# Kernel optimization log

Measured on AMD Instinct MI355X. Metric: run time of the kernel, lower is better.

## Reference

```python
import jax, jax.numpy as jnp
import numpy as np

B, V, C, D = 32, 64, 32, 256
VOCAB = 20000
NUM_T = 1000


def _run_lstm(x, Wih, Whh, b):
    # x: [T, B, H_in]; torch-style single-layer LSTM with zero initial state
    T, Bb, _ = x.shape
    H = Whh.shape[1]
    def step(carry, xt):
        h, c = carry
        z = xt @ Wih.T + h @ Whh.T + b
        i, f, g, o = jnp.split(z, 4, axis=-1)
        c = jax.nn.sigmoid(f) * c + jax.nn.sigmoid(i) * jnp.tanh(g)
        h = jax.nn.sigmoid(o) * jnp.tanh(c)
        return (h, c), h
    h0 = jnp.zeros((Bb, H), x.dtype)
    _, ys = jax.lax.scan(step, (h0, h0), x)
    return ys


def _forward(input_seqs, masks, lengths, seq_time_step, code_masks, emb, WQ1, WK1,
             decay, initial, lstm_Wih, lstm_Whh, lstm_b, hs_Wih, hs_Whh, hs_b,
             whk_W, whk_b, w1_W, w1_b, w2_W, w2_b, fuse_W, fuse_b, lab_W, lab_b,
             betas, Wdiff, diffusion_time_t, normal_noise):
    Bb, Vv, Cc = input_seqs.shape
    tok = input_seqs.reshape(-1, Cc)                      # [B*V, C]
    x = emb[tok]                                          # [B*V, C, D]
    q = x @ WQ1.T
    k = x @ WK1.T
    dp = jnp.einsum('bcd,bed->bce', q, k)                 # [B*V, C, C]
    cm = code_masks.reshape(-1, Cc)
    dp = dp - cm[:, None, :] - cm[:, :, None]
    sp = jax.nn.softmax(dp / jnp.sqrt(jnp.float32(D)), axis=-1)
    femb = jnp.einsum('bce,bed->bcd', sp, x)              # attended code embeddings
    femb = ((cm - 1e20) / -1e20)[:, :, None] * femb       # zero out padded codes
    dec = decay[tok][..., None]                           # [B*V, C, 1]
    ini = initial[tok][..., None]
    t = seq_time_step.reshape(-1)[:, None, None]          # [B*V, 1, 1]
    gate = jax.nn.sigmoid(dec * t + ini)                  # time-decay gate
    vv = jnp.einsum('bcx,bcd->bd', gate, femb)            # [B*V, D] visit vector
    vv = vv.reshape(Bb, Vv, -1).transpose(1, 0, 2)        # [V, B, D]

    lstm_out = _run_lstm(vv, lstm_Wih, lstm_Whh, lstm_b)  # [V, B, D]
    t_lstm = lstm_out.transpose(1, 0, 2)                  # [B, V, D]
    hiddenstate = _run_lstm(lstm_out, hs_Wih, hs_Whh, hs_b).transpose(1, 0, 2)

    # Vectorized form of the original per-step python loop.
    # NOTE: the original always uses e_k = t_lstm_out[:, 0:1, :] (step 0) -- kept faithfully.
    e_k = t_lstm[:, 0:1, :]                               # [B, 1, D]
    whp = hiddenstate[:, :-1, :] @ whk_W.T + whk_b        # [B, V-1, D]
    cat = jnp.concatenate([jnp.broadcast_to(e_k, whp.shape), whp], axis=-1)
    attn = jax.nn.softmax(jnp.tanh(cat @ w1_W.T + w1_b) @ w2_W.T + w2_b, axis=-1)
    rest = e_k * attn[..., 0:1] + whp * attn[..., 1:2]
    aligned = jnp.concatenate([e_k, rest], axis=1)        # [B, V, D]

    alpha = jnp.cumprod(1.0 - betas)[diffusion_time_t][:, None, None]
    noisy = aligned * jnp.sqrt(alpha) + normal_noise * jnp.sqrt(1.0 - alpha)
    predicted_noise = noisy @ Wdiff                       # surrogate for UNetModel (source not provided)
    gen = aligned + (normal_noise - predicted_noise)

    fused = jnp.concatenate([t_lstm, gen], axis=-1) @ fuse_W.T + fuse_b   # [B, V, D]
    mask_final = (jnp.arange(Vv)[None, :] == (lengths - 1)[:, None]).astype(fused.dtype)
    final = (fused * mask_final[:, :, None]).sum(axis=1)  # select last valid visit
    return final @ lab_W.T + lab_b                        # [B, 2]


def setup_inputs() -> dict:
    key = jax.random.key(0)
    ks = jax.random.split(key, 20)
    s = 0.05
    n = lambda i, shp: jax.random.normal(ks[i], shp, jnp.float32) * s
    emb = jax.random.normal(ks[0], (VOCAB + 1, D), jnp.float32) * 0.02
    emb = emb.at[VOCAB].set(0.0)  # padding_idx row
    return {
        'input_seqs': jax.random.randint(ks[1], (B, V, C), 0, VOCAB),
        'masks': jnp.zeros((B, V), jnp.float32),
        'lengths': jax.random.randint(ks[2], (B,), 1, V + 1),
        'seq_time_step': jax.random.uniform(ks[3], (B, V), jnp.float32),
        'code_masks': jnp.zeros((B, V, C), jnp.float32),
        'emb': emb,
        'WQ1': n(4, (D, D)), 'WK1': n(5, (D, D)),
        'decay': jnp.full((VOCAB + 1,), -0.1, jnp.float32),
        'initial': jnp.full((VOCAB + 1,), 1.0, jnp.float32),
        'lstm_Wih': n(6, (4 * D, D)), 'lstm_Whh': n(7, (4 * D, D)),
        'lstm_b': jnp.zeros((4 * D,), jnp.float32),
        'hs_Wih': n(8, (4 * D, D)), 'hs_Whh': n(9, (4 * D, D)),
        'hs_b': jnp.zeros((4 * D,), jnp.float32),
        'whk_W': n(10, (D, D)), 'whk_b': jnp.zeros((D,), jnp.float32),
        'w1_W': n(11, (64, 2 * D)), 'w1_b': jnp.zeros((64,), jnp.float32),
        'w2_W': n(12, (2, 64)), 'w2_b': jnp.zeros((2,), jnp.float32),
        'fuse_W': n(13, (D, 2 * D)), 'fuse_b': jnp.zeros((D,), jnp.float32),
        'lab_W': n(14, (2, D)), 'lab_b': jnp.zeros((2,), jnp.float32),
        'betas': jnp.linspace(1e-4, 0.02, NUM_T, dtype=jnp.float32),
        'Wdiff': n(15, (D, D)),
        'diffusion_time_t': jax.random.randint(ks[16], (B,), 0, NUM_T),
        'normal_noise': jax.random.normal(ks[17], (B, V, D), jnp.float32),
    }


def reference(input_seqs, masks, lengths, seq_time_step, code_masks, emb, WQ1, WK1,
              decay, initial, lstm_Wih, lstm_Whh, lstm_b, hs_Wih, hs_Whh, hs_b,
              whk_W, whk_b, w1_W, w1_b, w2_W, w2_b, fuse_W, fuse_b, lab_W, lab_b,
              betas, Wdiff, diffusion_time_t, normal_noise):
    return _forward(input_seqs, masks, lengths, seq_time_step, code_masks, emb, WQ1, WK1,
                    decay, initial, lstm_Wih, lstm_Whh, lstm_b, hs_Wih, hs_Whh, hs_b,
                    whk_W, whk_b, w1_W, w1_b, w2_W, w2_b, fuse_W, fuse_b, lab_W, lab_b,
                    betas, Wdiff, diffusion_time_t, normal_noise)
```

## Files before the change

kernel.cpp:

```cpp
#include <hip/hip_runtime.h>
#include <hip/hip_bf16.h>
#include <cmath>

typedef __attribute__((ext_vector_type(8))) short bf16x8;
typedef __attribute__((ext_vector_type(4))) float f32x4;
typedef __attribute__((ext_vector_type(4))) int i32x4;
typedef __attribute__((ext_vector_type(2))) unsigned int u32x2;

__device__ __forceinline__ float bf2f(unsigned short u) {
    unsigned int x = ((unsigned int)u) << 16;
    return __builtin_bit_cast(float, x);
}
__device__ __forceinline__ unsigned short f2bf(float f) {
    unsigned int x = __builtin_bit_cast(unsigned int, f);
    unsigned int lsb = (x >> 16) & 1u;
    x += 0x7fffu + lsb;
    return (unsigned short)(x >> 16);
}
__device__ __forceinline__ float sigm(float z) {
    return 1.f / (1.f + __expf(-z));
}
__device__ __forceinline__ float rcpf(float x) { return __builtin_amdgcn_rcpf(x); }
__device__ __forceinline__ float sigm_f(float z) { return rcpf(1.f + __expf(-z)); }
__device__ __forceinline__ float tanh_f(float z) { return 1.f - 2.f * rcpf(1.f + __expf(2.f * z)); }

__device__ __forceinline__ long ldg_sc8l(const void* p) {
    long r;
    asm volatile("global_load_dwordx2 %0, %1, off sc1" : "=v"(r) : "v"(p) : "memory");
    return r;
}
__device__ __forceinline__ u32x2 ldg_sc_u2(const void* p) {
    u32x2 r;
    asm volatile("global_load_dwordx2 %0, %1, off sc1" : "=v"(r) : "v"(p) : "memory");
    return r;
}
__device__ __forceinline__ void stg_sc_u2(void* p, u32x2 v) {
    asm volatile("global_store_dwordx2 %0, %1, off sc1" :: "v"(p), "v"(v) : "memory");
}
__device__ __forceinline__ void stg_sc_b(void* p, int v) {
    asm volatile("global_store_byte %0, %1, off sc1" :: "v"(p), "v"(v) : "memory");
}

__global__ void __launch_bounds__(256) pack_all(
    const float* __restrict__ Whh1, const float* __restrict__ Wih2,
    const float* __restrict__ Whh2, const float* __restrict__ Wih1,
    const float* __restrict__ WQ1, const float* __restrict__ WK1,
    const float* __restrict__ betas, const int* __restrict__ dift,
    const float* __restrict__ whk_W, const float* __restrict__ fuse_W,
    const float* __restrict__ w1_W,
    long* __restrict__ Wq, float* __restrict__ cs,
    unsigned short* __restrict__ W1h, unsigned short* __restrict__ M_pk,
    float* __restrict__ alpha, int* __restrict__ flags,
    float* __restrict__ whkT, float* __restrict__ fuseT,
    float* __restrict__ w1T) {
    int blk = blockIdx.x, tid = threadIdx.x;
    if (blk < 384) {
        int R = blk * 8 + (tid >> 5);
        int mat = R >> 10;
        int n = R & 1023;
        int t32 = tid & 31;
        const float* src = (mat == 0) ? Whh1 : (mat == 1 ? Wih2 : Whh2);
        const float* rp = src + (size_t)n * 256 + t32 * 8;
        float v[8];
        float mx = 0.f;
        for (int j = 0; j < 8; ++j) { v[j] = rp[j]; mx = fmaxf(mx, fabsf(v[j])); }
        for (int m = 1; m <= 16; m <<= 1) mx = fmaxf(mx, __shfl_xor(mx, m));
        float inv = mx > 0.f ? 127.f / mx : 0.f;
        unsigned int lo = 0, hi = 0;
        for (int j = 0; j < 4; ++j) {
            int iv = __float2int_rn(v[j] * inv);
            lo |= ((unsigned int)(unsigned char)(signed char)iv) << (8 * j);
            int iv2 = __float2int_rn(v[4 + j] * inv);
            hi |= ((unsigned int)(unsigned char)(signed char)iv2) << (8 * j);
        }
        int g = n >> 8, rem = n & 255;
        int w8 = rem >> 5, dt = (rem >> 4) & 1, cc = rem & 15;
        int t8 = g * 2 + dt;
        int kb = t32 >> 2, q = t32 & 3;
        unsigned int* dst = (unsigned int*)Wq +
            ((size_t)((mat * 512 + w8 * 64 + t8 * 8 + kb) * 64) + q * 16 + cc) * 2;
        dst[0] = lo;
        dst[1] = hi;
        if (t32 == 0) cs[mat * 1024 + n] = mx / 16129.f;
    } else if (blk < 512) {
        int cch = (blk - 384) * 256 + tid;
        int nt = cch >> 9;
        int r = cch & 511;
        int kb = r >> 6;
        int lane = r & 63;
        int grow = nt * 16 + (lane & 15);
        int k0 = kb * 32 + (lane >> 4) * 8;
        const float* sp = Wih1 + (size_t)grow * 256 + k0;
        bf16x8 hi;
        for (int j = 0; j < 8; ++j) hi[j] = (short)f2bf(sp[j]);
        *reinterpret_cast<bf16x8*>(W1h + (size_t)cch * 8) = hi;
    } else if (blk == 512) {
        if (tid < 32) {
            int tb = dift[tid];
            float p = 1.f;
            for (int i = 0; i <= tb; ++i) p *= (1.f - betas[i]);
            alpha[tid] = p;
        }
    } else if (blk == 513) {
        for (int i = tid; i < 2048; i += 256) flags[i] = 0;
    } else if (blk < 578) {
        int gid = (blk - 514) * 256 + tid;
        for (int i = 0; i < 4; ++i) {
            int e = gid + i * 16384;
            int k = e >> 8, dd = e & 255;
            whkT[e] = whk_W[(size_t)dd * 256 + k];
        }
    } else if (blk < 706) {
        int gid = (blk - 578) * 256 + tid;
        for (int i = 0; i < 4; ++i) {
            int e = gid + i * 32768;
            int k = e >> 8, dd = e & 255;
            fuseT[e] = fuse_W[(size_t)dd * 512 + k];
        }
    } else if (blk < 738) {
        int gid = (blk - 706) * 256 + tid;
        for (int i = 0; i < 4; ++i) {
            int e = gid + i * 8192;
            int k = e >> 6, j = e & 63;
            w1T[e] = w1_W[(size_t)j * 512 + k];
        }
    } else {
        __shared__ unsigned short As[256][32];
        __shared__ unsigned short Bs[256][32];
        int bx = blk - 738;
        int e0 = (bx >> 3) << 5;
        int f0 = (bx & 7) << 5;
        int col = tid & 31, rr = tid >> 5;
        for (int rep = 0; rep < 32; ++rep) {
            int d = rep * 8 + rr;
            As[d][col] = f2bf(WQ1[d * 256 + e0 + col]);
            Bs[d][col] = f2bf(WK1[d * 256 + f0 + col]);
        }
        __syncthreads();
        int el = tid & 31;
        int fl0 = tid >> 5;
        for (int i = 0; i < 4; ++i) {
            int fl = fl0 + 8 * i;
            float acc = 0.f;
            for (int d = 0; d < 256; ++d)
                acc += bf2f(As[d][el]) * bf2f(Bs[d][fl]);
            int e = e0 + el, f = f0 + fl;
            int kb = e >> 5, r = (e >> 3) & 3, j = e & 7;
            int nb = f >> 4;
            int lane = (r << 4) | (f & 15);
            M_pk[(((nb * 8 + kb) * 64) + lane) * 8 + j] = f2bf(acc);
        }
    }
}

__global__ void __launch_bounds__(256) attn_bags(
    const int* __restrict__ seqs, const float* __restrict__ tstep,
    const float* __restrict__ cmask, const float* __restrict__ emb,
    const float* __restrict__ decay, const float* __restrict__ initial,
    const unsigned short* __restrict__ M_pk, float* __restrict__ vv) {
    __shared__ __align__(16) unsigned short x_bf[32 * 256];
    __shared__ __align__(16) unsigned short t1_bf[32 * 256];
    __shared__ float dp_f[32 * 33];
    __shared__ float gate_sh[32];
    __shared__ float cm_sh[32];
    __shared__ int tok_sh[32];
    __shared__ float w_sh[32];

    int bag = blockIdx.x;
    int tid = threadIdx.x;

    if (tid < 32) {
        int tok = seqs[bag * 32 + tid];
        tok_sh[tid] = tok;
        float cm = cmask[bag * 32 + tid];
        cm_sh[tid] = cm;
        float tt = tstep[bag];
        float g = sigm(decay[tok] * tt + initial[tok]);
        g *= (cm - 1e20f) / (-1e20f);
        gate_sh[tid] = g;
    }
    __syncthreads();

    for (int it = 0; it < 8; ++it) {
        int fidx = it * 256 + tid;
        int c = fidx >> 6;
        int f4 = fidx & 63;
        const float4* src = reinterpret_cast<const float4*>(emb + (size_t)tok_sh[c] * 256) + f4;
        float4 vx = *src;
        int colx = f4 * 4;
        int eidx = c * 256 + (colx ^ ((c & 7) << 3));
        ushort4 w;
        w.x = f2bf(vx.x); w.y = f2bf(vx.y); w.z = f2bf(vx.z); w.w = f2bf(vx.w);
        *reinterpret_cast<ushort4*>(&x_bf[eidx]) = w;
    }
    __syncthreads();

    int wv = tid >> 6;
    int lane = tid & 63;
    int lr = lane & 15;
    int lk = lane >> 4;

    f32x4 acc[2][4];
    for (int a = 0; a < 2; ++a)
        for (int n = 0; n < 4; ++n) acc[a][n] = (f32x4){0.f, 0.f, 0.f, 0.f};
    for (int kb = 0; kb < 8; ++kb) {
        bf16x8 afr[2];
        for (int mb = 0; mb < 2; ++mb) {
            int row = mb * 16 + lr;
            int colx = kb * 32 + lk * 8;
            afr[mb] = *reinterpret_cast<const bf16x8*>(&x_bf[row * 256 + (colx ^ ((row & 7) << 3))]);
        }
        for (int nbi = 0; nbi < 4; ++nbi) {
            int nb = wv * 4 + nbi;
            bf16x8 bfr = *reinterpret_cast<const bf16x8*>(M_pk + (((nb * 8 + kb) * 64) + lane) * 8);
            acc[0][nbi] = __builtin_amdgcn_mfma_f32_16x16x32_bf16(afr[0], bfr, acc[0][nbi], 0, 0, 0);
            acc[1][nbi] = __builtin_amdgcn_mfma_f32_16x16x32_bf16(afr[1], bfr, acc[1][nbi], 0, 0, 0);
        }
    }
    for (int mb = 0; mb < 2; ++mb)
        for (int nbi = 0; nbi < 4; ++nbi)
            for (int r = 0; r < 4; ++r) {
                int row = mb * 16 + lk * 4 + r;
                int colx = wv * 64 + nbi * 16 + lr;
                t1_bf[row * 256 + (colx ^ ((row & 7) << 3))] = f2bf(acc[mb][nbi][r]);
            }
    __syncthreads();

    {
        int mb = wv >> 1, nb2 = wv & 1;
        f32x4 dacc = (f32x4){0.f, 0.f, 0.f, 0.f};
        for (int kb = 0; kb < 8; ++kb) {
            int cola = kb * 32 + lk * 8;
            int rowa = mb * 16 + lr;
            bf16x8 afr = *reinterpret_cast<const bf16x8*>(&t1_bf[rowa * 256 + (cola ^ ((rowa & 7) << 3))]);
            int rowb = nb2 * 16 + lr;
            bf16x8 bfr = *reinterpret_cast<const bf16x8*>(&x_bf[rowb * 256 + (cola ^ ((rowb & 7) << 3))]);
            dacc = __builtin_amdgcn_mfma_f32_16x16x32_bf16(afr, bfr, dacc, 0, 0, 0);
        }
        for (int r = 0; r < 4; ++r) {
            int c = mb * 16 + lk * 4 + r;
            int e = nb2 * 16 + lr;
            dp_f[c * 33 + e] = dacc[r];
        }
    }
    __syncthreads();

    if (tid < 32) {
        int c = tid;
        float cmc = cm_sh[c];
        float lg[32];
        float mx = -1e30f;
        for (int e = 0; e < 32; ++e) {
            float l = (dp_f[c * 33 + e] - cmc - cm_sh[e]) * 0.0625f;
            lg[e] = l;
            mx = fmaxf(mx, l);
        }
        float s = 0.f;
        for (int e = 0; e < 32; ++e) { float ex = __expf(lg[e] - mx); lg[e] = ex; s += ex; }
        float inv = 1.f / s;
        for (int e = 0; e < 32; ++e) dp_f[c * 33 + e] = lg[e] * inv;
    }
    __syncthreads();
    if (tid < 32) {
        int e = tid;
        float a2 = 0.f;
        for (int c = 0; c < 32; ++c) a2 += gate_sh[c] * dp_f[c * 33 + e];
        w_sh[e] = a2;
    }
    __syncthreads();

    float accv = 0.f;
    int d = tid;
    for (int e = 0; e < 32; ++e)
        accv += w_sh[e] * bf2f(x_bf[e * 256 + (d ^ ((e & 7) << 3))]);
    vv[(size_t)bag * 256 + d] = accv;
}

__global__ void __launch_bounds__(256) x1_mfma(const float* __restrict__ vv,
                                               const unsigned short* __restrict__ W1h,
                                               const float* __restrict__ lstm_b,
                                               unsigned short* __restrict__ X1bf) {
    __shared__ __align__(16) unsigned short xs[32 * 256];
    int blk = blockIdx.x;
    int rb = blk >> 3, gb = blk & 7;
    int tid = threadIdx.x;
    for (int it = 0; it < 8; ++it) {
        int idx = it * 256 + tid;
        int row = idx >> 6, f4 = idx & 63;
        float4 v = *reinterpret_cast<const float4*>(vv + (size_t)(rb * 32 + row) * 256 + f4 * 4);
        ushort4 w;
        w.x = f2bf(v.x); w.y = f2bf(v.y); w.z = f2bf(v.z); w.w = f2bf(v.w);
        *reinterpret_cast<ushort4*>(&xs[row * 256 + ((f4 * 4) ^ ((row & 7) << 3))]) = w;
    }
    __syncthreads();
    int wv = tid >> 6, lane = tid & 63, cl = lane & 15, kh = lane >> 4;
    f32x4 acc[2][2];
    for (int n = 0; n < 2; ++n) {
        int nt = gb * 8 + wv * 2 + n;
        float bz = lstm_b[nt * 16 + cl];
        acc[n][0] = (f32x4){bz, bz, bz, bz};
        acc[n][1] = (f32x4){bz, bz, bz, bz};
    }
    #pragma unroll
    for (int kb = 0; kb < 8; ++kb) {
        int k = kb * 32 + kh * 8;
        bf16x8 a0 = *reinterpret_cast<const bf16x8*>(&xs[cl * 256 + (k ^ ((cl & 7) << 3))]);
        bf16x8 a1 = *reinterpret_cast<const bf16x8*>(&xs[(16 + cl) * 256 + (k ^ (((16 + cl) & 7) << 3))]);
        for (int n = 0; n < 2; ++n) {
            int nt = gb * 8 + wv * 2 + n;
            size_t o = ((size_t)(nt * 8 + kb) * 64 + lane) * 8;
            bf16x8 bh = *reinterpret_cast<const bf16x8*>(W1h + o);
            acc[n][0] = __builtin_amdgcn_mfma_f32_16x16x32_bf16(a0, bh, acc[n][0], 0, 0, 0);
            acc[n][1] = __builtin_amdgcn_mfma_f32_16x16x32_bf16(a1, bh, acc[n][1], 0, 0, 0);
        }
    }
    for (int n = 0; n < 2; ++n) {
        int nt = gb * 8 + wv * 2 + n;
        int g = nt * 16 + cl;
        int dX = g & 255, gt = g >> 8;
        for (int mt = 0; mt < 2; ++mt)
            for (int r = 0; r < 4; ++r) {
                int row = rb * 32 + mt * 16 + kh * 4 + r;
                int b = row >> 6, t = row & 63;
                X1bf[((size_t)t * 32 + b) * 1024 + dX * 4 + gt] = f2bf(acc[n][mt][r]);
            }
    }
}

__global__ void __launch_bounds__(512, 2) lstm_persist(
    const long* __restrict__ Wq, const float* __restrict__ cs,
    const unsigned short* __restrict__ X1bf, const float* __restrict__ hs_b,
    unsigned short* __restrict__ h1bf, unsigned short* __restrict__ h2bf,
    signed char* h1q, unsigned short* p1, int* flags) {
    int role = blockIdx.x;
    int half = role & 1;
    int kind = role >> 1;
    int tid = threadIdx.x;
    int w = tid >> 6, lane = tid & 63, c = lane & 15, q = lane >> 4;

    long wt[64];
    #pragma unroll
    for (int t8 = 0; t8 < 8; ++t8)
        #pragma unroll
        for (int kb = 0; kb < 8; ++kb)
            wt[t8 * 8 + kb] = Wq[(size_t)((kind * 512 + w * 64 + t8 * 8 + kb) * 64) + lane];
    float csv[8];
    #pragma unroll
    for (int t8 = 0; t8 < 8; ++t8) {
        int g = t8 >> 1, dt = t8 & 1;
        csv[t8] = cs[kind * 1024 + g * 256 + w * 32 + dt * 16 + c];
    }

    if (kind == 0) {
        __shared__ signed char hq[2][16][272];
        float cstate[8] = {0.f, 0.f, 0.f, 0.f, 0.f, 0.f, 0.f, 0.f};
        int B0 = half * 16 + q * 4;
        int dbase = w * 32;
        for (int t = 0; t < 64; ++t) {
            ushort4 xv[8];
            #pragma unroll
            for (int dt = 0; dt < 2; ++dt)
                #pragma unroll
                for (int r = 0; r < 4; ++r) {
                    int B = B0 + r, d = dbase + dt * 16 + c;
                    xv[dt * 4 + r] = *reinterpret_cast<const ushort4*>(
                        X1bf + ((size_t)(t * 32 + B) * 1024 + d * 4));
                }
            i32x4 acc[8];
            #pragma unroll
            for (int i = 0; i < 8; ++i) acc[i] = (i32x4){0, 0, 0, 0};
            if (t > 0) {
                int pb = (t - 1) & 1;
                long a[8];
                #pragma unroll
                for (int kb = 0; kb < 8; ++kb)
                    a[kb] = *reinterpret_cast<const long*>(&hq[pb][c][kb * 32 + q * 8]);
                #pragma unroll
                for (int t8 = 0; t8 < 8; ++t8)
                    #pragma unroll
                    for (int kb = 0; kb < 8; ++kb)
                        acc[t8] = __builtin_amdgcn_mfma_i32_16x16x32_i8(
                            a[kb], wt[t8 * 8 + kb], acc[t8], 0, 0, 0);
            }
            #pragma unroll
            for (int dt = 0; dt < 2; ++dt)
                #pragma unroll
                for (int r = 0; r < 4; ++r) {
                    int idx = dt * 4 + r;
                    ushort4 x = xv[idx];
                    float zi = (float)acc[0 + dt][r] * csv[0 + dt] + bf2f(x.x);
                    float zf = (float)acc[2 + dt][r] * csv[2 + dt] + bf2f(x.y);
                    float zg = (float)acc[4 + dt][r] * csv[4 + dt] + bf2f(x.z);
                    float zo = (float)acc[6 + dt][r] * csv[6 + dt] + bf2f(x.w);
                    float cn = sigm_f(zf) * cstate[idx] + sigm_f(zi) * tanh_f(zg);
                    float hn = sigm_f(zo) * tanh_f(cn);
                    cstate[idx] = cn;
                    int B = B0 + r, d = dbase + dt * 16 + c;
                    h1bf[(size_t)(t * 32 + B) * 256 + d] = f2bf(hn);
                    int hv = __float2int_rn(hn * 127.f);
                    hq[t & 1][q * 4 + r][d] = (signed char)hv;
                    stg_sc_b(h1q + (size_t)(t * 32 + B) * 256 + d, hv);
                }
            asm volatile("s_waitcnt vmcnt(0)" ::: "memory");
            if (lane == 0)
                __hip_atomic_store(flags + t * 16 + half * 8 + w, 1,
                                   __ATOMIC_RELAXED, __HIP_MEMORY_SCOPE_AGENT);
            __syncthreads();
        }
    } else if (kind == 1) {
        for (int s = 0; s < 64; ++s) {
            const int* f = flags + s * 16 + half * 8;
            while (1) {
                int v = 1;
                if (lane < 8)
                    v = __hip_atomic_load(f + lane, __ATOMIC_RELAXED, __HIP_MEMORY_SCOPE_AGENT);
                if (__all(v != 0)) break;
                __builtin_amdgcn_s_sleep(1);
            }
            __builtin_amdgcn_sched_barrier(0);
            const signed char* hb = h1q + (size_t)(s * 32 + half * 16) * 256;
            long a[8];
            #pragma unroll
            for (int kb = 0; kb < 8; ++kb)
                a[kb] = ldg_sc8l(hb + c * 256 + kb * 32 + q * 8);
            asm volatile("s_waitcnt vmcnt(0)" ::: "memory");
            __builtin_amdgcn_sched_barrier(0);
            i32x4 acc[8];
            #pragma unroll
            for (int i = 0; i < 8; ++i) acc[i] = (i32x4){0, 0, 0, 0};
            #pragma unroll
            for (int t8 = 0; t8 < 8; ++t8)
                #pragma unroll
                for (int kb = 0; kb < 8; ++kb)
                    acc[t8] = __builtin_amdgcn_mfma_i32_16x16x32_i8(
                        a[kb], wt[t8 * 8 + kb], acc[t8], 0, 0, 0);
            #pragma unroll
            for (int t8 = 0; t8 < 8; ++t8) {
                int g = t8 >> 1, dt = t8 & 1;
                int n = g * 256 + w * 32 + dt * 16 + c;
                u32x2 pv;
                pv.x = (unsigned int)f2bf((float)acc[t8][0] * csv[t8]) |
                       ((unsigned int)f2bf((float)acc[t8][1] * csv[t8]) << 16);
                pv.y = (unsigned int)f2bf((float)acc[t8][2] * csv[t8]) |
                       ((unsigned int)f2bf((float)acc[t8][3] * csv[t8]) << 16);
                stg_sc_u2(p1 + ((size_t)(s * 2 + half) * 1024 + n) * 16 + q * 4, pv);
            }
            asm volatile("s_waitcnt vmcnt(0)" ::: "memory");
            if (lane == 0)
                __hip_atomic_store(flags + 1024 + s * 16 + half * 8 + w, 1,
                                   __ATOMIC_RELAXED, __HIP_MEMORY_SCOPE_AGENT);
        }
    } else {
        __shared__ signed char hq2[2][16][272];
        float cstate[8] = {0.f, 0.f, 0.f, 0.f, 0.f, 0.f, 0.f, 0.f};
        float bias[8];
        #pragma unroll
        for (int t8 = 0; t8 < 8; ++t8) {
            int g = t8 >> 1, dt = t8 & 1;
            bias[t8] = hs_b[g * 256 + w * 32 + dt * 16 + c];
        }
        int B0 = half * 16 + q * 4;
        int dbase = w * 32;
        for (int s = 0; s < 64; ++s) {
            const int* fp = flags + 1024 + s * 16 + half * 8 + w;
            while (__hip_atomic_load(fp, __ATOMIC_RELAXED, __HIP_MEMORY_SCOPE_AGENT) == 0)
                __builtin_amdgcn_s_sleep(1);
            __builtin_amdgcn_sched_barrier(0);
            u32x2 pv[8];
            #pragma unroll
            for (int t8 = 0; t8 < 8; ++t8) {
                int g = t8 >> 1, dt = t8 & 1;
                int n = g * 256 + w * 32 + dt * 16 + c;
                pv[t8] = ldg_sc_u2(p1 + ((size_t)(s * 2 + half) * 1024 + n) * 16 + q * 4);
            }
            i32x4 acc[8];
            #pragma unroll
            for (int i = 0; i < 8; ++i) acc[i] = (i32x4){0, 0, 0, 0};
            if (s > 0) {
                int pb = (s - 1) & 1;
                long a[8];
                #pragma unroll
                for (int kb = 0; kb < 8; ++kb)
                    a[kb] = *reinterpret_cast<const long*>(&hq2[pb][c][kb * 32 + q * 8]);
                asm volatile("s_waitcnt vmcnt(0)" ::: "memory");
                __builtin_amdgcn_sched_barrier(0);
                #pragma unroll
                for (int t8 = 0; t8 < 8; ++t8)
                    #pragma unroll
                    for (int kb = 0; kb < 8; ++kb)
                        acc[t8] = __builtin_amdgcn_mfma_i32_16x16x32_i8(
                            a[kb], wt[t8 * 8 + kb], acc[t8], 0, 0, 0);
            } else {
                asm volatile("s_waitcnt vmcnt(0)" ::: "memory");
                __builtin_amdgcn_sched_barrier(0);
            }
            #pragma unroll
            for (int dt = 0; dt < 2; ++dt)
                #pragma unroll
                for (int r = 0; r < 4; ++r) {
                    int idx = dt * 4 + r;
                    float p_i = bf2f((unsigned short)((r < 2 ? pv[0 + dt].x : pv[0 + dt].y) >> ((r & 1) * 16)));
                    float p_f = bf2f((unsigned short)((r < 2 ? pv[2 + dt].x : pv[2 + dt].y) >> ((r & 1) * 16)));
                    float p_g = bf2f((unsigned short)((r < 2 ? pv[4 + dt].x : pv[4 + dt].y) >> ((r & 1) * 16)));
                    float p_o = bf2f((unsigned short)((r < 2 ? pv[6 + dt].x : pv[6 + dt].y) >> ((r & 1) * 16)));
                    float zi = (float)acc[0 + dt][r] * csv[0 + dt] + p_i + bias[0 + dt];
                    float zf = (float)acc[2 + dt][r] * csv[2 + dt] + p_f + bias[2 + dt];
                    float zg = (float)acc[4 + dt][r] * csv[4 + dt] + p_g + bias[4 + dt];
                    float zo = (float)acc[6 + dt][r] * csv[6 + dt] + p_o + bias[6 + dt];
                    float cn = sigm_f(zf) * cstate[idx] + sigm_f(zi) * tanh_f(zg);
                    float hn = sigm_f(zo) * tanh_f(cn);
                    cstate[idx] = cn;
                    int B = B0 + r, d = dbase + dt * 16 + c;
                    h2bf[(size_t)(s * 32 + B) * 256 + d] = f2bf(hn);
                    hq2[s & 1][q * 4 + r][d] = (signed char)__float2int_rn(hn * 127.f);
                }
            __syncthreads();
        }
    }
}

__global__ void __launch_bounds__(256) tail_k(
    const int* __restrict__ lengths,
    const unsigned short* __restrict__ h1, const unsigned short* __restrict__ h2,
    const float* __restrict__ whkT, const float* __restrict__ whk_b,
    const float* __restrict__ w1T, const float* __restrict__ w1_b,
    const float* __restrict__ w2_W, const float* __restrict__ w2_b,
    const float* __restrict__ fuseT, const float* __restrict__ fuse_b,
    const float* __restrict__ lab_W, const float* __restrict__ lab_b,
    const float* __restrict__ Wdiff, const float* __restrict__ alpha,
    const float* __restrict__ noise, float* __restrict__ out) {
    __shared__ float ek[256], tv[256], hs[256], whp[256], a1s[64];
    __shared__ float noisy_s[256], fin[512], fused_s[256], attn_s[2];
    int b = blockIdx.x, tid = threadIdx.x;
    int vstar = lengths[b] - 1;
    {
        ek[tid] = bf2f(h1[(size_t)b * 256 + tid]);
        tv[tid] = bf2f(h1[((size_t)vstar * 32 + b) * 256 + tid]);
        if (vstar > 0)
            hs[tid] = bf2f(h2[((size_t)(vstar - 1) * 32 + b) * 256 + tid]);
    }
    __syncthreads();

    float aligned;
    if (vstar > 0) {
        float s0 = 0.f, s1 = 0.f, s2 = 0.f, s3 = 0.f;
        for (int k = 0; k < 256; k += 4) {
            s0 += whkT[(k + 0) * 256 + tid] * hs[k + 0];
            s1 += whkT[(k + 1) * 256 + tid] * hs[k + 1];
            s2 += whkT[(k + 2) * 256 + tid] * hs[k + 2];
            s3 += whkT[(k + 3) * 256 + tid] * hs[k + 3];
        }
        whp[tid] = whk_b[tid] + s0 + s1 + s2 + s3;
        __syncthreads();
        if (tid < 64) {
            float a0 = 0.f, a1 = 0.f, a2 = 0.f, a3 = 0.f;
            for (int k = 0; k < 256; k += 4) {
                a0 += w1T[(k + 0) * 64 + tid] * ek[k + 0];
                a1 += w1T[(k + 1) * 64 + tid] * ek[k + 1];
                a2 += w1T[(k + 2) * 64 + tid] * ek[k + 2];
                a3 += w1T[(k + 3) * 64 + tid] * ek[k + 3];
            }
            for (int k = 0; k < 256; k += 4) {
                a0 += w1T[(256 + k + 0) * 64 + tid] * whp[k + 0];
                a1 += w1T[(256 + k + 1) * 64 + tid] * whp[k + 1];
                a2 += w1T[(256 + k + 2) * 64 + tid] * whp[k + 2];
                a3 += w1T[(256 + k + 3) * 64 + tid] * whp[k + 3];
            }
            a1s[tid] = tanhf(w1_b[tid] + a0 + a1 + a2 + a3);
        }
        __syncthreads();
        if (tid < 2) {
            float a3 = w2_b[tid];
            const float* wr2 = w2_W + tid * 64;
            for (int k = 0; k < 64; ++k) a3 += wr2[k] * a1s[k];
            attn_s[tid] = a3;
        }
        __syncthreads();
        float m = fmaxf(attn_s[0], attn_s[1]);
        float e0 = __expf(attn_s[0] - m), e1 = __expf(attn_s[1] - m);
        float inv = 1.f / (e0 + e1);
        aligned = ek[tid] * (e0 * inv) + whp[tid] * (e1 * inv);
    } else {
        aligned = ek[tid];
    }

    float al = alpha[b];
    float sa = sqrtf(al), sb = sqrtf(1.f - al);
    float nz = noise[((size_t)b * 64 + vstar) * 256 + tid];
    noisy_s[tid] = aligned * sa + nz * sb;
    __syncthreads();
    {
        float p0 = 0.f, p1v = 0.f, p2 = 0.f, p3 = 0.f;
        for (int k = 0; k < 256; k += 4) {
            p0 += noisy_s[k + 0] * Wdiff[(size_t)(k + 0) * 256 + tid];
            p1v += noisy_s[k + 1] * Wdiff[(size_t)(k + 1) * 256 + tid];
            p2 += noisy_s[k + 2] * Wdiff[(size_t)(k + 2) * 256 + tid];
            p3 += noisy_s[k + 3] * Wdiff[(size_t)(k + 3) * 256 + tid];
        }
        float gen = aligned + nz - (p0 + p1v + p2 + p3);
        fin[tid] = tv[tid];
        fin[256 + tid] = gen;
    }
    __syncthreads();
    {
        float f0 = 0.f, f1 = 0.f, f2 = 0.f, f3 = 0.f;
        for (int k = 0; k < 512; k += 4) {
            f0 += fuseT[(k + 0) * 256 + tid] * fin[k + 0];
            f1 += fuseT[(k + 1) * 256 + tid] * fin[k + 1];
            f2 += fuseT[(k + 2) * 256 + tid] * fin[k + 2];
            f3 += fuseT[(k + 3) * 256 + tid] * fin[k + 3];
        }
        fused_s[tid] = fuse_b[tid] + f0 + f1 + f2 + f3;
    }
    __syncthreads();
    if (tid < 2) {
        float o = lab_b[tid];
        const float* lw = lab_W + tid * 256;
        for (int k = 0; k < 256; ++k) o += lw[k] * fused_s[k];
        out[b * 2 + tid] = o;
    }
}

extern "C" void kernel_launch(void* const* d_in, const int* in_sizes, int n_in,
                              void* d_out, int out_size, void* d_ws, size_t ws_size,
                              hipStream_t stream) {
    const int*   seqs    = (const int*)  d_in[0];
    const int*   lengths = (const int*)  d_in[2];
    const float* tstep   = (const float*)d_in[3];
    const float* cmask   = (const float*)d_in[4];
    const float* emb     = (const float*)d_in[5];
    const float* WQ1     = (const float*)d_in[6];
    const float* WK1     = (const float*)d_in[7];
    const float* decay   = (const float*)d_in[8];
    const float* initial = (const float*)d_in[9];
    const float* Wih1    = (const float*)d_in[10];
    const float* Whh1    = (const float*)d_in[11];
    const float* lstm_b  = (const float*)d_in[12];
    const float* Wih2    = (const float*)d_in[13];
    const float* Whh2    = (const float*)d_in[14];
    const float* hs_b    = (const float*)d_in[15];
    const float* whk_W   = (const float*)d_in[16];
    const float* whk_b   = (const float*)d_in[17];
    const float* w1_W    = (const float*)d_in[18];
    const float* w1_b    = (const float*)d_in[19];
    const float* w2_W    = (const float*)d_in[20];
    const float* w2_b    = (const float*)d_in[21];
    const float* fuse_W  = (const float*)d_in[22];
    const float* fuse_b  = (const float*)d_in[23];
    const float* lab_W   = (const float*)d_in[24];
    const float* lab_b   = (const float*)d_in[25];
    const float* betas   = (const float*)d_in[26];
    const float* Wdiff   = (const float*)d_in[27];
    const int*   dift    = (const int*)  d_in[28];
    const float* noise   = (const float*)d_in[29];
    float* out = (float*)d_out;

    float* ws = (float*)d_ws;
    size_t off = 0;
    auto alloc = [&](size_t nfloats) { size_t r = off; off += (nfloats + 63) & ~(size_t)63; return r; };
    unsigned short* M_pk  = (unsigned short*)(ws + alloc(32768));
    float*          alpha = ws + alloc(64);
    float*          cs    = ws + alloc(3072);
    int*            flags = (int*)(ws + alloc(2048));
    float*          vv    = ws + alloc(524288);
    unsigned short* X1bf  = (unsigned short*)(ws + alloc(1048576));
    unsigned short* h1bf  = (unsigned short*)(ws + alloc(262144));
    unsigned short* h2bf  = (unsigned short*)(ws + alloc(262144));
    unsigned short* p1    = (unsigned short*)(ws + alloc(1048576));
    long*           Wq    = (long*)(ws + alloc(196608));
    unsigned short* W1h   = (unsigned short*)(ws + alloc(131072));
    float*          whkT  = ws + alloc(65536);
    float*          fuseT = ws + alloc(131072);
    float*          w1T   = ws + alloc(32768);
    signed char*    h1q   = (signed char*)vv;

    pack_all<<<802, 256, 0, stream>>>(Whh1, Wih2, Whh2, Wih1, WQ1, WK1, betas, dift,
                                      whk_W, fuse_W, w1_W,
                                      Wq, cs, W1h, M_pk, alpha, flags,
                                      whkT, fuseT, w1T);
    attn_bags<<<2048, 256, 0, stream>>>(seqs, tstep, cmask, emb, decay, initial, M_pk, vv);
    x1_mfma<<<512, 256, 0, stream>>>(vv, W1h, lstm_b, X1bf);
    lstm_persist<<<6, 512, 0, stream>>>(Wq, cs, X1bf, hs_b, h1bf, h2bf, h1q, p1, flags);
    tail_k<<<32, 256, 0, stream>>>(lengths, h1bf, h2bf, whkT, whk_b,
                                   w1T, w1_b, w2_W, w2_b, fuseT, fuse_b,
                                   lab_W, lab_b, Wdiff, alpha, noise, out);
}
```

Measured before the change: 340.9 us.

## Precompute vocab-projected embeddings and coarsen LSTM pipeline flags with packed stores

A new eprep kernel multiplies the whole embedding table (20001 rows) by M_pk once, and attn_bags then gathers the projected rows instead of running its own MFMA per bag. The persistent LSTM kernel switches to one block-wide flag per step instead of per-wave flags. The second-stage producer handles two timesteps per flag, and h1q/h1bf/h2bf are written with packed stores built through lane shuffles rather than byte and short stores. This trades about 2048×32 gathered rows of compute for a full-vocab GEMM and reduces flag polling and store count, at the cost of extra __syncthreads and coarser pipeline granularity.

```diff
diff --git a/kernel.cpp b/kernel.cpp
--- a/kernel.cpp
+++ b/kernel.cpp
@@ -36,9 +36,6 @@
 }
 __device__ __forceinline__ void stg_sc_u2(void* p, u32x2 v) {
     asm volatile("global_store_dwordx2 %0, %1, off sc1" :: "v"(p), "v"(v) : "memory");
-}
-__device__ __forceinline__ void stg_sc_b(void* p, int v) {
-    asm volatile("global_store_byte %0, %1, off sc1" :: "v"(p), "v"(v) : "memory");
 }
 
 __global__ void __launch_bounds__(256) pack_all(
@@ -102,7 +99,7 @@
             alpha[tid] = p;
         }
     } else if (blk == 513) {
-        for (int i = tid; i < 2048; i += 256) flags[i] = 0;
+        for (int i = tid; i < 4096; i += 256) flags[i] = 0;
     } else if (blk < 578) {
         int gid = (blk - 514) * 256 + tid;
         for (int i = 0; i < 4; ++i) {
@@ -153,11 +150,59 @@
     }
 }
 
+__global__ void __launch_bounds__(256) eprep(const float* __restrict__ emb,
+                                             const unsigned short* __restrict__ M_pk,
+                                             unsigned short* __restrict__ Ep) {
+    __shared__ __align__(16) unsigned short x_bf[32 * 256];
+    int v0 = blockIdx.x * 32;
+    int tid = threadIdx.x;
+    for (int it = 0; it < 8; ++it) {
+        int fidx = it * 256 + tid;
+        int cc = fidx >> 6;
+        int f4 = fidx & 63;
+        int row = v0 + cc;
+        float4 vx = make_float4(0.f, 0.f, 0.f, 0.f);
+        if (row < 20001)
+            vx = *(reinterpret_cast<const float4*>(emb + (size_t)row * 256) + f4);
+        int colx = f4 * 4;
+        ushort4 w;
+        w.x = f2bf(vx.x); w.y = f2bf(vx.y); w.z = f2bf(vx.z); w.w = f2bf(vx.w);
+        *reinterpret_cast<ushort4*>(&x_bf[cc * 256 + (colx ^ ((cc & 7) << 3))]) = w;
+    }
+    __syncthreads();
+    int wv = tid >> 6, lane = tid & 63, lr = lane & 15, lk = lane >> 4;
+    f32x4 acc[2][4];
+    for (int a = 0; a < 2; ++a)
+        for (int n = 0; n < 4; ++n) acc[a][n] = (f32x4){0.f, 0.f, 0.f, 0.f};
+    for (int kb = 0; kb < 8; ++kb) {
+        bf16x8 afr[2];
+        for (int mb = 0; mb < 2; ++mb) {
+            int row = mb * 16 + lr;
+            int colx = kb * 32 + lk * 8;
+            afr[mb] = *reinterpret_cast<const bf16x8*>(&x_bf[row * 256 + (colx ^ ((row & 7) << 3))]);
+        }
+        for (int nbi = 0; nbi < 4; ++nbi) {
+            int nb = wv * 4 + nbi;
+            bf16x8 bfr = *reinterpret_cast<const bf16x8*>(M_pk + (((nb * 8 + kb) * 64) + lane) * 8);
+            acc[0][nbi] = __builtin_amdgcn_mfma_f32_16x16x32_bf16(afr[0], bfr, acc[0][nbi], 0, 0, 0);
+            acc[1][nbi] = __builtin_amdgcn_mfma_f32_16x16x32_bf16(afr[1], bfr, acc[1][nbi], 0, 0, 0);
+        }
+    }
+    for (int mb = 0; mb < 2; ++mb)
+        for (int nbi = 0; nbi < 4; ++nbi)
+            for (int r = 0; r < 4; ++r) {
+                int row = mb * 16 + lk * 4 + r;
+                int col = wv * 64 + nbi * 16 + lr;
+                if (v0 + row < 20001)
+                    Ep[(size_t)(v0 + row) * 256 + col] = f2bf(acc[mb][nbi][r]);
+            }
+}
+
 __global__ void __launch_bounds__(256) attn_bags(
     const int* __restrict__ seqs, const float* __restrict__ tstep,
     const float* __restrict__ cmask, const float* __restrict__ emb,
     const float* __restrict__ decay, const float* __restrict__ initial,
-    const unsigned short* __restrict__ M_pk, float* __restrict__ vv) {
+    const unsigned short* __restrict__ Ep, float* __restrict__ vv) {
     __shared__ __align__(16) unsigned short x_bf[32 * 256];
     __shared__ __align__(16) unsigned short t1_bf[32 * 256];
     __shared__ float dp_f[32 * 33];
@@ -193,38 +238,19 @@
         w.x = f2bf(vx.x); w.y = f2bf(vx.y); w.z = f2bf(vx.z); w.w = f2bf(vx.w);
         *reinterpret_cast<ushort4*>(&x_bf[eidx]) = w;
     }
+    for (int it = 0; it < 4; ++it) {
+        int idx = it * 256 + tid;
+        int cc = idx >> 5;
+        int colx = (idx & 31) * 8;
+        bf16x8 e = *reinterpret_cast<const bf16x8*>(Ep + (size_t)tok_sh[cc] * 256 + colx);
+        *reinterpret_cast<bf16x8*>(&t1_bf[cc * 256 + (colx ^ ((cc & 7) << 3))]) = e;
+    }
     __syncthreads();
 
     int wv = tid >> 6;
     int lane = tid & 63;
     int lr = lane & 15;
     int lk = lane >> 4;
-
-    f32x4 acc[2][4];
-    for (int a = 0; a < 2; ++a)
-        for (int n = 0; n < 4; ++n) acc[a][n] = (f32x4){0.f, 0.f, 0.f, 0.f};
-    for (int kb = 0; kb < 8; ++kb) {
-        bf16x8 afr[2];
-        for (int mb = 0; mb < 2; ++mb) {
-            int row = mb * 16 + lr;
-            int colx = kb * 32 + lk * 8;
-            afr[mb] = *reinterpret_cast<const bf16x8*>(&x_bf[row * 256 + (colx ^ ((row & 7) << 3))]);
-        }
-        for (int nbi = 0; nbi < 4; ++nbi) {
-            int nb = wv * 4 + nbi;
-            bf16x8 bfr = *reinterpret_cast<const bf16x8*>(M_pk + (((nb * 8 + kb) * 64) + lane) * 8);
-            acc[0][nbi] = __builtin_amdgcn_mfma_f32_16x16x32_bf16(afr[0], bfr, acc[0][nbi], 0, 0, 0);
-            acc[1][nbi] = __builtin_amdgcn_mfma_f32_16x16x32_bf16(afr[1], bfr, acc[1][nbi], 0, 0, 0);
-        }
-    }
-    for (int mb = 0; mb < 2; ++mb)
-        for (int nbi = 0; nbi < 4; ++nbi)
-            for (int r = 0; r < 4; ++r) {
-                int row = mb * 16 + lk * 4 + r;
-                int colx = wv * 64 + nbi * 16 + lr;
-                t1_bf[row * 256 + (colx ^ ((row & 7) << 3))] = f2bf(acc[mb][nbi][r]);
-            }
-    __syncthreads();
 
     {
         int mb = wv >> 1, nb2 = wv & 1;
@@ -361,11 +387,9 @@
             #pragma unroll
             for (int dt = 0; dt < 2; ++dt)
                 #pragma unroll
-                for (int r = 0; r < 4; ++r) {
-                    int B = B0 + r, d = dbase + dt * 16 + c;
+                for (int r = 0; r < 4; ++r)
                     xv[dt * 4 + r] = *reinterpret_cast<const ushort4*>(
-                        X1bf + ((size_t)(t * 32 + B) * 1024 + d * 4));
-                }
+                        X1bf + ((size_t)(t * 32 + B0 + r) * 1024 + (dbase + dt * 16 + c) * 4));
             i32x4 acc[8];
             #pragma unroll
             for (int i = 0; i < 8; ++i) acc[i] = (i32x4){0, 0, 0, 0};
@@ -382,6 +406,8 @@
                         acc[t8] = __builtin_amdgcn_mfma_i32_16x16x32_i8(
                             a[kb], wt[t8 * 8 + kb], acc[t8], 0, 0, 0);
             }
+            float hnv[8];
+            unsigned int hvb[8];
             #pragma unroll
             for (int dt = 0; dt < 2; ++dt)
                 #pragma unroll
@@ -395,59 +421,86 @@
                     float cn = sigm_f(zf) * cstate[idx] + sigm_f(zi) * tanh_f(zg);
                     float hn = sigm_f(zo) * tanh_f(cn);
                     cstate[idx] = cn;
-                    int B = B0 + r, d = dbase + dt * 16 + c;
-                    h1bf[(size_t)(t * 32 + B) * 256 + d] = f2bf(hn);
+                    hnv[idx] = hn;
                     int hv = __float2int_rn(hn * 127.f);
-                    hq[t & 1][q * 4 + r][d] = (signed char)hv;
-                    stg_sc_b(h1q + (size_t)(t * 32 + B) * 256 + d, hv);
+                    hq[t & 1][q * 4 + r][dbase + dt * 16 + c] = (signed char)hv;
+                    hvb[idx] = (unsigned int)(unsigned char)(signed char)hv;
                 }
-            asm volatile("s_waitcnt vmcnt(0)" ::: "memory");
-            if (lane == 0)
-                __hip_atomic_store(flags + t * 16 + half * 8 + w, 1,
+            #pragma unroll
+            for (int dt = 0; dt < 2; ++dt)
+                #pragma unroll
+                for (int r = 0; r < 4; ++r) {
+                    unsigned int b = hvb[dt * 4 + r];
+                    unsigned int p = (unsigned int)__shfl_xor((int)b, 1);
+                    unsigned int pair = (c & 1) ? (p | (b << 8)) : (b | (p << 8));
+                    unsigned int pq = (unsigned int)__shfl_xor((int)pair, 2);
+                    unsigned int quad = (c & 2) ? (pq | (pair << 16)) : (pair | (pq << 16));
+                    unsigned int oh = (unsigned int)__shfl_xor((int)quad, 4);
+                    if ((c & 7) == 0) {
+                        u32x2 v8;
+                        v8.x = quad; v8.y = oh;
+                        stg_sc_u2(h1q + (size_t)(t * 32 + B0 + r) * 256 + dbase + dt * 16 + c, v8);
+                    }
+                }
+            #pragma unroll
+            for (int dt = 0; dt < 2; ++dt)
+                #pragma unroll
+                for (int r = 0; r < 4; ++r) {
+                    unsigned int ph = f2bf(hnv[dt * 4 + r]);
+                    unsigned int pp = (unsigned int)__shfl_xor((int)ph, 1);
+                    if (!(c & 1))
+                        *reinterpret_cast<unsigned int*>(
+                            h1bf + (size_t)(t * 32 + B0 + r) * 256 + dbase + dt * 16 + c) =
+                            ph | (pp << 16);
+                }
+            __syncthreads();
+            if (tid == 0)
+                __hip_atomic_store(flags + (t * 2 + half) * 16, 1,
                                    __ATOMIC_RELAXED, __HIP_MEMORY_SCOPE_AGENT);
-            __syncthreads();
         }
     } else if (kind == 1) {
-        for (int s = 0; s < 64; ++s) {
-            const int* f = flags + s * 16 + half * 8;
-            while (1) {
-                int v = 1;
-                if (lane < 8)
-                    v = __hip_atomic_load(f + lane, __ATOMIC_RELAXED, __HIP_MEMORY_SCOPE_AGENT);
-                if (__all(v != 0)) break;
+        for (int s2 = 0; s2 < 64; s2 += 2) {
+            const int* fp = flags + ((s2 + 1) * 2 + half) * 16;
+            while (__hip_atomic_load(fp, __ATOMIC_RELAXED, __HIP_MEMORY_SCOPE_AGENT) == 0)
                 __builtin_amdgcn_s_sleep(1);
-            }
             __builtin_amdgcn_sched_barrier(0);
-            const signed char* hb = h1q + (size_t)(s * 32 + half * 16) * 256;
-            long a[8];
-            #pragma unroll
-            for (int kb = 0; kb < 8; ++kb)
-                a[kb] = ldg_sc8l(hb + c * 256 + kb * 32 + q * 8);
+            const signed char* hb0 = h1q + (size_t)(s2 * 32 + half * 16) * 256;
+            const signed char* hb1 = h1q + (size_t)((s2 + 1) * 32 + half * 16) * 256;
+            long a[8], b[8];
+            #pragma unroll
+            for (int kb = 0; kb < 8; ++kb) {
+                a[kb] = ldg_sc8l(hb0 + c * 256 + kb * 32 + q * 8);
+                b[kb] = ldg_sc8l(hb1 + c * 256 + kb * 32 + q * 8);
+            }
             asm volatile("s_waitcnt vmcnt(0)" ::: "memory");
             __builtin_amdgcn_sched_barrier(0);
-            i32x4 acc[8];
-            #pragma unroll
-            for (int i = 0; i < 8; ++i) acc[i] = (i32x4){0, 0, 0, 0};
-            #pragma unroll
-            for (int t8 = 0; t8 < 8; ++t8)
-                #pragma unroll
-                for (int kb = 0; kb < 8; ++kb)
-                    acc[t8] = __builtin_amdgcn_mfma_i32_16x16x32_i8(
-                        a[kb], wt[t8 * 8 + kb], acc[t8], 0, 0, 0);
-            #pragma unroll
-            for (int t8 = 0; t8 < 8; ++t8) {
-                int g = t8 >> 1, dt = t8 & 1;
-                int n = g * 256 + w * 32 + dt * 16 + c;
-                u32x2 pv;
-                pv.x = (unsigned int)f2bf((float)acc[t8][0] * csv[t8]) |
-                       ((unsigned int)f2bf((float)acc[t8][1] * csv[t8]) << 16);
-                pv.y = (unsigned int)f2bf((float)acc[t8][2] * csv[t8]) |
-                       ((unsigned int)f2bf((float)acc[t8][3] * csv[t8]) << 16);
-                stg_sc_u2(p1 + ((size_t)(s * 2 + half) * 1024 + n) * 16 + q * 4, pv);
-            }
-            asm volatile("s_waitcnt vmcnt(0)" ::: "memory");
-            if (lane == 0)
-                __hip_atomic_store(flags + 1024 + s * 16 + half * 8 + w, 1,
+            #pragma unroll
+            for (int step = 0; step < 2; ++step) {
+                int s = s2 + step;
+                i32x4 acc[8];
+                #pragma unroll
+                for (int i = 0; i < 8; ++i) acc[i] = (i32x4){0, 0, 0, 0};
+                #pragma unroll
+                for (int t8 = 0; t8 < 8; ++t8)
+                    #pragma unroll
+                    for (int kb = 0; kb < 8; ++kb)
+                        acc[t8] = __builtin_amdgcn_mfma_i32_16x16x32_i8(
+                            step ? b[kb] : a[kb], wt[t8 * 8 + kb], acc[t8], 0, 0, 0);
+                #pragma unroll
+                for (int t8 = 0; t8 < 8; ++t8) {
+                    int g = t8 >> 1, dt = t8 & 1;
+                    int n = g * 256 + w * 32 + dt * 16 + c;
+                    u32x2 pv;
+                    pv.x = (unsigned int)f2bf((float)acc[t8][0] * csv[t8]) |
+                           ((unsigned int)f2bf((float)acc[t8][1] * csv[t8]) << 16);
+                    pv.y = (unsigned int)f2bf((float)acc[t8][2] * csv[t8]) |
+                           ((unsigned int)f2bf((float)acc[t8][3] * csv[t8]) << 16);
+                    stg_sc_u2(p1 + ((size_t)(s * 2 + half) * 1024 + n) * 16 + q * 4, pv);
+                }
+            }
+            __syncthreads();
+            if (tid == 0)
+                __hip_atomic_store(flags + 2048 + ((s2 >> 1) * 2 + half) * 16, 1,
                                    __ATOMIC_RELAXED, __HIP_MEMORY_SCOPE_AGENT);
         }
     } else {
@@ -462,10 +515,12 @@
         int B0 = half * 16 + q * 4;
         int dbase = w * 32;
         for (int s = 0; s < 64; ++s) {
-            const int* fp = flags + 1024 + s * 16 + half * 8 + w;
-            while (__hip_atomic_load(fp, __ATOMIC_RELAXED, __HIP_MEMORY_SCOPE_AGENT) == 0)
-                __builtin_amdgcn_s_sleep(1);
-            __builtin_amdgcn_sched_barrier(0);
+            if ((s & 1) == 0) {
+                const int* fp = flags + 2048 + ((s >> 1) * 2 + half) * 16;
+                while (__hip_atomic_load(fp, __ATOMIC_RELAXED, __HIP_MEMORY_SCOPE_AGENT) == 0)
+                    __builtin_amdgcn_s_sleep(1);
+                __builtin_amdgcn_sched_barrier(0);
+            }
             u32x2 pv[8];
             #pragma unroll
             for (int t8 = 0; t8 < 8; ++t8) {
@@ -494,6 +549,7 @@
                 asm volatile("s_waitcnt vmcnt(0)" ::: "memory");
                 __builtin_amdgcn_sched_barrier(0);
             }
+            float hnv[8];
             #pragma unroll
             for (int dt = 0; dt < 2; ++dt)
                 #pragma unroll
@@ -510,9 +566,19 @@
                     float cn = sigm_f(zf) * cstate[idx] + sigm_f(zi) * tanh_f(zg);
                     float hn = sigm_f(zo) * tanh_f(cn);
                     cstate[idx] = cn;
-                    int B = B0 + r, d = dbase + dt * 16 + c;
-                    h2bf[(size_t)(s * 32 + B) * 256 + d] = f2bf(hn);
-                    hq2[s & 1][q * 4 + r][d] = (signed char)__float2int_rn(hn * 127.f);
+                    hnv[idx] = hn;
+                    hq2[s & 1][q * 4 + r][dbase + dt * 16 + c] = (signed char)__float2int_rn(hn * 127.f);
+                }
+            #pragma unroll
+            for (int dt = 0; dt < 2; ++dt)
+                #pragma unroll
+                for (int r = 0; r < 4; ++r) {
+                    unsigned int ph = f2bf(hnv[dt * 4 + r]);
+                    unsigned int pp = (unsigned int)__shfl_xor((int)ph, 1);
+                    if (!(c & 1))
+                        *reinterpret_cast<unsigned int*>(
+                            h2bf + (size_t)(s * 32 + B0 + r) * 256 + dbase + dt * 16 + c) =
+                            ph | (pp << 16);
                 }
             __syncthreads();
         }
@@ -661,7 +727,7 @@
     unsigned short* M_pk  = (unsigned short*)(ws + alloc(32768));
     float*          alpha = ws + alloc(64);
     float*          cs    = ws + alloc(3072);
-    int*            flags = (int*)(ws + alloc(2048));
+    int*            flags = (int*)(ws + alloc(4096));
     float*          vv    = ws + alloc(524288);
     unsigned short* X1bf  = (unsigned short*)(ws + alloc(1048576));
     unsigned short* h1bf  = (unsigned short*)(ws + alloc(262144));
@@ -672,13 +738,15 @@
     float*          whkT  = ws + alloc(65536);
     float*          fuseT = ws + alloc(131072);
     float*          w1T   = ws + alloc(32768);
-    signed char*    h1q   = (signed char*)vv;
+    signed char*    h1q   = (signed char*)(ws + alloc(131072));
+    unsigned short* Ep    = (unsigned short*)(ws + alloc(2560128));
 
     pack_all<<<802, 256, 0, stream>>>(Whh1, Wih2, Whh2, Wih1, WQ1, WK1, betas, dift,
                                       whk_W, fuse_W, w1_W,
                                       Wq, cs, W1h, M_pk, alpha, flags,
                                       whkT, fuseT, w1T);
-    attn_bags<<<2048, 256, 0, stream>>>(seqs, tstep, cmask, emb, decay, initial, M_pk, vv);
+    eprep<<<626, 256, 0, stream>>>(emb, M_pk, Ep);
+    attn_bags<<<2048, 256, 0, stream>>>(seqs, tstep, cmask, emb, decay, initial, Ep, vv);
     x1_mfma<<<512, 256, 0, stream>>>(vv, W1h, lstm_b, X1bf);
     lstm_persist<<<6, 512, 0, stream>>>(Wq, cs, X1bf, hs_b, h1bf, h2bf, h1q, p1, flags);
     tail_k<<<32, 256, 0, stream>>>(lengths, h1bf, h2bf, whkT, whk_b,
```

Result: slower. 373.4 us (+9.5%).
